# Kernel tuning notes

Hardware: AMD Instinct MI355X
Metric: run time of the kernel (lower is better)

The kernel has to match this reference:

```python
import jax, jax.numpy as jnp
import numpy as np

# Model dims (match init_kwargs)
B, S = 2, 2048          # batch, seq_len
H = 1024                # hidden_size
D = 2048                # expert_hidden_dim
E = 8                   # num_experts
K = 2                   # num_experts_per_tok (top_k)


def setup_inputs() -> dict:
    key = jax.random.key(0)
    k_x, k_g, k_w1, k_w2 = jax.random.split(key, 4)
    x = jax.random.normal(k_x, (B, S, H), jnp.float32)
    # router gate: Linear(H, E, bias=False)
    gate_w = jax.random.normal(k_g, (H, E), jnp.float32) / jnp.sqrt(H).astype(jnp.float32)
    # per-expert FFN params stacked on leading expert axis
    W1 = jax.random.normal(k_w1, (E, H, D), jnp.float32) / jnp.sqrt(H).astype(jnp.float32)
    b1 = jnp.zeros((E, D), jnp.float32)
    W2 = jax.random.normal(k_w2, (E, D, H), jnp.float32) / jnp.sqrt(D).astype(jnp.float32)
    b2 = jnp.zeros((E, H), jnp.float32)
    return {"x": x, "gate_w": gate_w, "W1": W1, "b1": b1, "W2": W2, "b2": b2}


def reference(x, gate_w, W1, b1, W2, b2):
    # --- router ---
    logits = jnp.einsum('bsh,he->bse', x, gate_w)            # [B,S,E]
    probs = jax.nn.softmax(logits, axis=-1)                  # [B,S,E]
    topk_p, idx = jax.lax.top_k(probs, K)                    # [B,S,K] each
    topk_p = topk_p / topk_p.sum(axis=-1, keepdims=True)     # renormalize over top-k
    one_hot = jax.nn.one_hot(idx, E, dtype=probs.dtype)      # [B,S,K,E]
    # combine weight per (token, expert); topk indices are distinct so this
    # equals the original's masked-sum of router_probs_flat * expert_mask
    combine = jnp.einsum('bske,bsk->bse', one_hot, topk_p)   # [B,S,E]

    # --- aux load-balancing loss (faithful to original reductions) ---
    tokens_per_expert = one_hot.sum(axis=-2).mean(axis=0)    # [S,E]
    avg_prob_per_expert = probs.mean(axis=(0, 1))            # [E]
    aux_loss = E * (tokens_per_expert * avg_prob_per_expert).sum()

    # --- experts: dense-equivalent of gather-FFN-scatter (tokens with
    # combine weight 0 contribute 0, matching the masked loop) ---
    out = jnp.zeros_like(x)
    for e in range(E):  # fixed small loop over structurally distinct experts
        h = jax.nn.gelu(jnp.einsum('bsh,hd->bsd', x, W1[e]) + b1[e], approximate=False)
        out = out + combine[..., e:e + 1] * (jnp.einsum('bsd,dh->bsh', h, W2[e]) + b2[e])
    return out, aux_loss
```

## Files before the change

### kernel.cpp

```cpp
#include <hip/hip_runtime.h>
#include <hip/hip_bf16.h>

#define NTOK 4096
#define HD   1024
#define DD   2048
#define NE   8
#define SLOTS (2*NTOK)

typedef unsigned short u16;
typedef unsigned int   u32;
typedef __attribute__((ext_vector_type(8))) __bf16 bf16x8;
typedef __attribute__((ext_vector_type(4))) float  f32x4;

__device__ __forceinline__ float bf2f(u16 u) {
    u32 v = ((u32)u) << 16;
    return __uint_as_float(v);
}
__device__ __forceinline__ u16 f2bf(float f) {
    __hip_bfloat16 h = __float2bfloat16(f);
    return *reinterpret_cast<u16*>(&h);
}

__device__ __forceinline__ void gload_lds16(const void* g, void* l) {
    __builtin_amdgcn_global_load_lds(
        (__attribute__((address_space(1))) void*)g,
        (__attribute__((address_space(3))) void*)l,
        16, 0, 0);
}

__device__ __forceinline__ float gelu_f(float v) {
    float x = 0.7978845608028654f * (v + 0.044715f * v * v * v);
    float e = exp2f(x * 2.8853900817779268f);
    float th = 1.f - 2.f * __builtin_amdgcn_rcpf(e + 1.f);
    return 0.5f * v * (1.f + th);
}

__global__ __launch_bounds__(256) void cvt2_k(
        const float* __restrict__ W1, const float* __restrict__ W2,
        u16* __restrict__ W1t, u16* __restrict__ W2t) {
    int z = blockIdx.z;
    const float* src; u16* dst; int R, C;
    if (z < NE) { src = W1 + (size_t)z * HD * DD;        dst = W1t + (size_t)z * HD * DD;        R = HD; C = DD; }
    else        { src = W2 + (size_t)(z - NE) * DD * HD; dst = W2t + (size_t)(z - NE) * DD * HD; R = DD; C = HD; }
    int tcols = C >> 6;
    int r0 = (blockIdx.x / tcols) * 64;
    int c0 = (blockIdx.x % tcols) * 64;

    __shared__ u16 tile[64][68];
    int tid = threadIdx.x;
    int rr  = tid >> 4;
    int cc4 = (tid & 15) * 4;
#pragma unroll
    for (int j = 0; j < 4; ++j) {
        int r = rr + j * 16;
        float4 v = *reinterpret_cast<const float4*>(src + (size_t)(r0 + r) * C + c0 + cc4);
        tile[r][cc4 + 0] = f2bf(v.x); tile[r][cc4 + 1] = f2bf(v.y);
        tile[r][cc4 + 2] = f2bf(v.z); tile[r][cc4 + 3] = f2bf(v.w);
    }
    __syncthreads();
    int cc = tid >> 3, sl = tid & 7;
#pragma unroll
    for (int p = 0; p < 2; ++p) {
        int c = p * 32 + cc;
        u16 tmp[8];
#pragma unroll
        for (int k = 0; k < 8; ++k) tmp[k] = tile[sl * 8 + k][c];
        *reinterpret_cast<uint4*>(dst + (size_t)(c0 + c) * R + r0 + sl * 8) =
            *reinterpret_cast<uint4*>(tmp);
    }
}

__global__ __launch_bounds__(256) void router_k(
        const float* __restrict__ x, const float* __restrict__ gw,
        u16* __restrict__ xb,
        int* __restrict__ counts, float* __restrict__ sum_probs,
        int* __restrict__ tk_idx, float* __restrict__ tk_w) {
    __shared__ int   bcnt[NE];
    __shared__ float bprob[NE];
    int tid = threadIdx.x;
    if (tid < NE) { bcnt[tid] = 0; bprob[tid] = 0.f; }
    __syncthreads();

    int gtid = blockIdx.x * 256 + tid;
    int t    = gtid >> 6;
    int lane = gtid & 63;

    float acc[NE] = {0.f,0.f,0.f,0.f,0.f,0.f,0.f,0.f};
    const float* xr = x + (size_t)t * HD;
    u16* xbr = xb + (size_t)t * HD;
#pragma unroll
    for (int i = 0; i < HD / 64; ++i) {
        int h = lane + i * 64;
        float xv = xr[h];
        xbr[h] = f2bf(xv);
        const float4* g = reinterpret_cast<const float4*>(gw + (size_t)h * NE);
        float4 g0 = g[0], g1 = g[1];
        acc[0] = fmaf(xv, g0.x, acc[0]); acc[1] = fmaf(xv, g0.y, acc[1]);
        acc[2] = fmaf(xv, g0.z, acc[2]); acc[3] = fmaf(xv, g0.w, acc[3]);
        acc[4] = fmaf(xv, g1.x, acc[4]); acc[5] = fmaf(xv, g1.y, acc[5]);
        acc[6] = fmaf(xv, g1.z, acc[6]); acc[7] = fmaf(xv, g1.w, acc[7]);
    }
#pragma unroll
    for (int off = 32; off >= 1; off >>= 1) {
#pragma unroll
        for (int e = 0; e < NE; ++e) acc[e] += __shfl_xor(acc[e], off);
    }
    float m = acc[0];
#pragma unroll
    for (int e = 1; e < NE; ++e) m = fmaxf(m, acc[e]);
    float p[NE]; float s = 0.f;
#pragma unroll
    for (int e = 0; e < NE; ++e) { p[e] = expf(acc[e] - m); s += p[e]; }
    float inv = 1.f / s;

    int i1 = 0; float v1 = p[0];
#pragma unroll
    for (int e = 1; e < NE; ++e) if (p[e] > v1) { v1 = p[e]; i1 = e; }
    int i2 = -1; float v2 = -1.f;
#pragma unroll
    for (int e = 0; e < NE; ++e) if (e != i1 && p[e] > v2) { v2 = p[e]; i2 = e; }
    float wsum = v1 + v2;

    if (lane < NE) atomicAdd(&bprob[lane], p[lane] * inv);
    if (lane == 0) {
        atomicAdd(&bcnt[i1], 1);
        atomicAdd(&bcnt[i2], 1);
        tk_idx[2 * t]     = i1;  tk_idx[2 * t + 1] = i2;
        tk_w[2 * t]       = v1 / wsum;
        tk_w[2 * t + 1]   = v2 / wsum;
    }
    __syncthreads();
    if (tid < NE) {
        if (bcnt[tid]) atomicAdd(&counts[tid], bcnt[tid]);
        atomicAdd(&sum_probs[tid], bprob[tid]);
    }
}

__global__ __launch_bounds__(256) void scatter_k(
        const int* __restrict__ tk_idx, const int* __restrict__ counts,
        int* __restrict__ cursor, int* __restrict__ slot_tok,
        int* __restrict__ inv_slot, int* __restrict__ offsets) {
    __shared__ int off[NE];
    if (threadIdx.x == 0) {
        int o = 0;
        for (int e = 0; e < NE; ++e) { off[e] = o; o += counts[e]; }
        if (blockIdx.x == 0)
            for (int e = 0; e < NE; ++e) offsets[e] = off[e];
    }
    __syncthreads();
    int t = blockIdx.x * 256 + threadIdx.x;
    if (t >= NTOK) return;
#pragma unroll
    for (int k = 0; k < 2; ++k) {
        int e = tk_idx[2 * t + k];
        int pos = atomicAdd(&cursor[e], 1);
        int s = off[e] + pos;
        slot_tok[s] = t;
        inv_slot[2 * t + k] = s;
    }
}

template<int KD, bool GATHER, bool GELU>
__global__ __launch_bounds__(256) void gemm_dense_k(
        const u16* __restrict__ A,
        const u16* __restrict__ Bt,
        const float* __restrict__ bias,
        const int* __restrict__ counts, const int* __restrict__ offsets,
        const int* __restrict__ slot_tok,
        u16* __restrict__ outb, int ND) {
    int mb = blockIdx.y;
    int e = -1, m0 = 0, accb = 0;
#pragma unroll
    for (int ee = 0; ee < NE; ++ee) {
        int nb = (counts[ee] + 127) >> 7;
        if (e < 0 && mb < accb + nb) { e = ee; m0 = (mb - accb) * 128; }
        accb += nb;
    }
    if (e < 0) return;
    int cnt = counts[e], base = offsets[e];
    int n0 = blockIdx.x * 128;

    __shared__ u16 As[128 * 64];
    __shared__ u16 Bs[128 * 64];
    __shared__ int ids[128];

    int tid  = threadIdx.x;
    int lane = tid & 63;
    int w    = tid >> 6;
    int wr   = w >> 1, wc = w & 1;
    int lrow = lane & 15, khi = lane >> 4;

    if constexpr (GATHER) {
        if (tid < 128) ids[tid] = (m0 + tid < cnt) ? slot_tok[base + m0 + tid] : 0;
    }
    __syncthreads();

    const u16* Bte = Bt + (size_t)e * (size_t)ND * KD;
    int srow = tid >> 3;
    int sslot = tid & 7;

    const u16 *gA[4], *gB[4];
#pragma unroll
    for (int j = 0; j < 4; ++j) {
        int r = j * 32 + srow;
        size_t gr;
        if constexpr (GATHER) gr = (size_t)ids[r];
        else                  gr = (size_t)(base + m0 + r);
        gA[j] = A   + gr * KD                + ((sslot ^ (r & 7)) << 3);
        gB[j] = Bte + (size_t)(n0 + r) * KD  + ((sslot ^ (r & 7)) << 3);
    }

    f32x4 acc[4][4];
#pragma unroll
    for (int m = 0; m < 4; ++m)
#pragma unroll
        for (int n = 0; n < 4; ++n) acc[m][n] = {0.f, 0.f, 0.f, 0.f};

    constexpr int NK = KD / 64;
#pragma unroll 1
    for (int t = 0; t < NK; ++t) {
#pragma unroll
        for (int j = 0; j < 4; ++j) {
            gload_lds16(gA[j] + t * 64, (char*)As + j * 4096 + tid * 16);
            gload_lds16(gB[j] + t * 64, (char*)Bs + j * 4096 + tid * 16);
        }
        __syncthreads();
#pragma unroll
        for (int ks = 0; ks < 2; ++ks) {
            int slot = ks * 4 + khi;
            bf16x8 af[4], bv[4];
#pragma unroll
            for (int m = 0; m < 4; ++m) {
                int r = wr * 64 + m * 16 + lrow;
                af[m] = *reinterpret_cast<const bf16x8*>(
                    &As[r * 64 + ((slot ^ (r & 7)) << 3)]);
            }
#pragma unroll
            for (int n = 0; n < 4; ++n) {
                int r = wc * 64 + n * 16 + lrow;
                bv[n] = *reinterpret_cast<const bf16x8*>(
                    &Bs[r * 64 + ((slot ^ (r & 7)) << 3)]);
            }
            __builtin_amdgcn_s_setprio(1);
#pragma unroll
            for (int m = 0; m < 4; ++m)
#pragma unroll
                for (int n = 0; n < 4; ++n)
                    acc[m][n] = __builtin_amdgcn_mfma_f32_16x16x32_bf16(
                        af[m], bv[n], acc[m][n], 0, 0, 0);
            __builtin_amdgcn_s_setprio(0);
        }
        __syncthreads();
    }

    constexpr int PST = 72;
    u16* patch = As + w * 16 * PST;
    float bvals[4];
    if constexpr (GELU) {
#pragma unroll
        for (int n = 0; n < 4; ++n)
            bvals[n] = bias[(size_t)e * ND + n0 + wc * 64 + n * 16 + lrow];
    }
#pragma unroll
    for (int m = 0; m < 4; ++m) {
#pragma unroll
        for (int n = 0; n < 4; ++n)
#pragma unroll
            for (int i = 0; i < 4; ++i) {
                float v = acc[m][n][i];
                if constexpr (GELU) {
                    v += bvals[n];
                    v = gelu_f(v);
                }
                patch[(khi * 4 + i) * PST + n * 16 + lrow] = f2bf(v);
            }
        __syncthreads();
        int prow = lane >> 3, sl = lane & 7;
#pragma unroll
        for (int p = 0; p < 2; ++p) {
            int row  = p * 8 + prow;
            uint4 q = *reinterpret_cast<const uint4*>(&patch[row * PST + sl * 8]);
            int grow = m0 + wr * 64 + m * 16 + row;
            if (grow < cnt)
                *reinterpret_cast<uint4*>(
                    outb + (size_t)(base + grow) * ND + n0 + wc * 64 + sl * 8) = q;
        }
        __syncthreads();
    }
}

template<int KD, bool GATHER, bool GELU>
__global__ __launch_bounds__(512) void gemm_big2_k(
        const u16* __restrict__ A,
        const u16* __restrict__ Bt,
        const float* __restrict__ bias,
        const int* __restrict__ counts, const int* __restrict__ offsets,
        const int* __restrict__ slot_tok,
        u16* __restrict__ outb, int ND) {
    int mb = blockIdx.y;
    int e = -1, m0 = 0, accb = 0;
#pragma unroll
    for (int ee = 0; ee < NE; ++ee) {
        int nb = (counts[ee] + 255) >> 8;
        if (e < 0 && mb < accb + nb) { e = ee; m0 = (mb - accb) * 256; }
        accb += nb;
    }
    if (e < 0) return;
    int cnt = counts[e], base = offsets[e];
    int n0 = blockIdx.x * 128;

    __shared__ u16 As[2][256 * 64];
    __shared__ u16 Bs[2][128 * 64];
    __shared__ int ids[256];

    int tid  = threadIdx.x;
    int lane = tid & 63;
    int w    = tid >> 6;
    int wr   = w >> 1, wc = w & 1;
    int lrow = lane & 15, khi = lane >> 4;

    if constexpr (GATHER) {
        if (tid < 256) ids[tid] = (m0 + tid < cnt) ? slot_tok[base + m0 + tid] : 0;
    }
    __syncthreads();

    const u16* Bte = Bt + (size_t)e * (size_t)ND * KD;
    int srow = tid >> 3;
    int sslot = tid & 7;

    const u16 *gA[4], *gB[2];
#pragma unroll
    for (int j = 0; j < 4; ++j) {
        int r = j * 64 + srow;
        size_t gr;
        if constexpr (GATHER) gr = (size_t)ids[r];
        else                  gr = (size_t)(base + m0 + r);
        gA[j] = A + gr * KD + ((sslot ^ (r & 7)) << 3);
    }
#pragma unroll
    for (int j = 0; j < 2; ++j) {
        int r = j * 64 + srow;
        gB[j] = Bte + (size_t)(n0 + r) * KD + ((sslot ^ (r & 7)) << 3);
    }

    f32x4 acc[4][4];
#pragma unroll
    for (int m = 0; m < 4; ++m)
#pragma unroll
        for (int n = 0; n < 4; ++n) acc[m][n] = {0.f, 0.f, 0.f, 0.f};

    auto stage = [&](int buf, int t) {
#pragma unroll
        for (int j = 0; j < 4; ++j)
            gload_lds16(gA[j] + t * 64, (char*)As[buf] + j * 8192 + tid * 16);
#pragma unroll
        for (int j = 0; j < 2; ++j)
            gload_lds16(gB[j] + t * 64, (char*)Bs[buf] + j * 8192 + tid * 16);
    };
    auto compute = [&](int buf) {
#pragma unroll
        for (int ks = 0; ks < 2; ++ks) {
            int slot = ks * 4 + khi;
            bf16x8 af[4], bv[4];
#pragma unroll
            for (int m = 0; m < 4; ++m) {
                int r = wr * 64 + m * 16 + lrow;
                af[m] = *reinterpret_cast<const bf16x8*>(
                    &As[buf][r * 64 + ((slot ^ (r & 7)) << 3)]);
            }
#pragma unroll
            for (int n = 0; n < 4; ++n) {
                int r = wc * 64 + n * 16 + lrow;
                bv[n] = *reinterpret_cast<const bf16x8*>(
                    &Bs[buf][r * 64 + ((slot ^ (r & 7)) << 3)]);
            }
            __builtin_amdgcn_s_setprio(1);
#pragma unroll
            for (int m = 0; m < 4; ++m)
#pragma unroll
                for (int n = 0; n < 4; ++n)
                    acc[m][n] = __builtin_amdgcn_mfma_f32_16x16x32_bf16(
                        af[m], bv[n], acc[m][n], 0, 0, 0);
            __builtin_amdgcn_s_setprio(0);
        }
    };

    constexpr int NK = KD / 64;
    stage(0, 0);
    __syncthreads();
#pragma unroll 1
    for (int t = 0; t < NK; ++t) {
        if (t + 1 < NK) stage((t + 1) & 1, t + 1);
        compute(t & 1);
        __syncthreads();
    }

    constexpr int PST = 72;
    u16* patch = ((u16*)As) + w * 16 * PST;
    float bvals[4];
    if constexpr (GELU) {
#pragma unroll
        for (int n = 0; n < 4; ++n)
            bvals[n] = bias[(size_t)e * ND + n0 + wc * 64 + n * 16 + lrow];
    }
#pragma unroll
    for (int m = 0; m < 4; ++m) {
#pragma unroll
        for (int n = 0; n < 4; ++n)
#pragma unroll
            for (int i = 0; i < 4; ++i) {
                float v = acc[m][n][i];
                if constexpr (GELU) {
                    v += bvals[n];
                    v = gelu_f(v);
                }
                patch[(khi * 4 + i) * PST + n * 16 + lrow] = f2bf(v);
            }
        __syncthreads();
        int prow = lane >> 3, sl = lane & 7;
#pragma unroll
        for (int p = 0; p < 2; ++p) {
            int row  = p * 8 + prow;
            uint4 q = *reinterpret_cast<const uint4*>(&patch[row * PST + sl * 8]);
            int grow = m0 + wr * 64 + m * 16 + row;
            if (grow < cnt)
                *reinterpret_cast<uint4*>(
                    outb + (size_t)(base + grow) * ND + n0 + wc * 64 + sl * 8) = q;
        }
        __syncthreads();
    }
}

__global__ __launch_bounds__(256) void combine_k(
        const int* __restrict__ tk_idx, const float* __restrict__ tk_w,
        const int* __restrict__ inv_slot, const u16* __restrict__ ybuf,
        const float* __restrict__ b2, float* __restrict__ out) {
    int gtid = blockIdx.x * 256 + threadIdx.x;
    int t = gtid >> 6;
    int lane = gtid & 63;
    int e0 = tk_idx[2 * t], e1 = tk_idx[2 * t + 1];
    float w0 = tk_w[2 * t], w1 = tk_w[2 * t + 1];
    int s0 = inv_slot[2 * t], s1 = inv_slot[2 * t + 1];

#pragma unroll
    for (int i = 0; i < 2; ++i) {
        int c = lane * 8 + i * 512;
        uint4 q0 = *reinterpret_cast<const uint4*>(ybuf + (size_t)s0 * HD + c);
        uint4 q1 = *reinterpret_cast<const uint4*>(ybuf + (size_t)s1 * HD + c);
        float y0[8] = {bf2f((u16)(q0.x&0xffff)), bf2f((u16)(q0.x>>16)),
                       bf2f((u16)(q0.y&0xffff)), bf2f((u16)(q0.y>>16)),
                       bf2f((u16)(q0.z&0xffff)), bf2f((u16)(q0.z>>16)),
                       bf2f((u16)(q0.w&0xffff)), bf2f((u16)(q0.w>>16))};
        float y1[8] = {bf2f((u16)(q1.x&0xffff)), bf2f((u16)(q1.x>>16)),
                       bf2f((u16)(q1.y&0xffff)), bf2f((u16)(q1.y>>16)),
                       bf2f((u16)(q1.z&0xffff)), bf2f((u16)(q1.z>>16)),
                       bf2f((u16)(q1.w&0xffff)), bf2f((u16)(q1.w>>16))};
        float r[8];
#pragma unroll
        for (int j = 0; j < 8; ++j) {
            float v0 = y0[j] + b2[e0 * HD + c + j];
            float v1 = y1[j] + b2[e1 * HD + c + j];
            r[j] = w0 * v0 + w1 * v1;
        }
        float* op = out + (size_t)t * HD + c;
        *reinterpret_cast<float4*>(op)     = make_float4(r[0], r[1], r[2], r[3]);
        *reinterpret_cast<float4*>(op + 4) = make_float4(r[4], r[5], r[6], r[7]);
    }
}

__global__ void finalize_k(const int* __restrict__ counts,
                           const float* __restrict__ sum_probs,
                           float* __restrict__ out_aux) {
    if (threadIdx.x == 0) {
        double s = 0.0;
        for (int e = 0; e < NE; ++e) s += (double)counts[e] * (double)sum_probs[e];
        out_aux[0] = (float)(s * (8.0 / (2.0 * (double)NTOK)));
    }
}

extern "C" void kernel_launch(void* const* d_in, const int* in_sizes, int n_in,
                              void* d_out, int out_size, void* d_ws, size_t ws_size,
                              hipStream_t stream) {
    const float* x   = (const float*)d_in[0];
    const float* gw  = (const float*)d_in[1];
    const float* W1  = (const float*)d_in[2];
    const float* b1  = (const float*)d_in[3];
    const float* W2  = (const float*)d_in[4];
    const float* b2  = (const float*)d_in[5];
    float* out = (float*)d_out;

    char* ws = (char*)d_ws;
    int*   counts    = (int*)(ws + 0);
    int*   cursor    = (int*)(ws + 32);
    int*   offsets   = (int*)(ws + 64);
    float* sum_probs = (float*)(ws + 128);
    int*   tk_idx    = (int*)(ws + 512);
    float* tk_w      = (float*)(ws + 33280);
    int*   slot_tok  = (int*)(ws + 66048);
    int*   inv_slot  = (int*)(ws + 98816);
    u16*   xb        = (u16*)(ws + 131584);
    u16*   W1t       = (u16*)(ws + 8520192);
    u16*   W2t       = (u16*)(ws + 42074624);
    u16*   hbuf      = (u16*)(ws + 75629056);
    u16*   ybuf      = W1t;

    hipMemsetAsync(ws, 0, 512, stream);

    cvt2_k<<<dim3(512, 1, 2 * NE), 256, 0, stream>>>(W1, W2, W1t, W2t);
    router_k<<<NTOK / 4, 256, 0, stream>>>(x, gw, xb, counts, sum_probs, tk_idx, tk_w);
    scatter_k<<<NTOK / 256, 256, 0, stream>>>(tk_idx, counts, cursor,
                                              slot_tok, inv_slot, offsets);

    gemm_dense_k<HD, true, true><<<dim3(DD / 128, 72, 1), 256, 0, stream>>>(
        xb, W1t, b1, counts, offsets, slot_tok, hbuf, DD);
    gemm_big2_k<DD, false, false><<<dim3(HD / 128, 40, 1), 512, 0, stream>>>(
        hbuf, W2t, nullptr, counts, offsets, slot_tok, ybuf, HD);

    combine_k<<<NTOK / 4, 256, 0, stream>>>(tk_idx, tk_w, inv_slot, ybuf, b2, out);
    finalize_k<<<1, 64, 0, stream>>>(counts, sum_probs, out + (size_t)NTOK * HD);
}
```

Before: 247.1 us.

## Replace second expert GEMM with smaller 128x64 single-buffered tile kernel

The second expert GEMM moves from 256x128 tiles with 512 threads and double-buffered LDS to 128x64 tiles with 256 threads and a single LDS buffer. The grid grows from 40x8 to 72x16 blocks, giving more blocks to fill the GPU's compute units. The cost is lower data reuse per block and no overlap of global loads with MFMA work. The separate finalize kernel is also folded into combine_k to save one launch.

```diff
diff --git a/kernel.cpp b/kernel.cpp
--- a/kernel.cpp
+++ b/kernel.cpp
@@ -289,29 +289,26 @@
     }
 }
 
-template<int KD, bool GATHER, bool GELU>
-__global__ __launch_bounds__(512) void gemm_big2_k(
+template<int KD>
+__global__ __launch_bounds__(256) void gemm_n64_k(
         const u16* __restrict__ A,
         const u16* __restrict__ Bt,
-        const float* __restrict__ bias,
         const int* __restrict__ counts, const int* __restrict__ offsets,
-        const int* __restrict__ slot_tok,
         u16* __restrict__ outb, int ND) {
     int mb = blockIdx.y;
     int e = -1, m0 = 0, accb = 0;
 #pragma unroll
     for (int ee = 0; ee < NE; ++ee) {
-        int nb = (counts[ee] + 255) >> 8;
-        if (e < 0 && mb < accb + nb) { e = ee; m0 = (mb - accb) * 256; }
+        int nb = (counts[ee] + 127) >> 7;
+        if (e < 0 && mb < accb + nb) { e = ee; m0 = (mb - accb) * 128; }
         accb += nb;
     }
     if (e < 0) return;
     int cnt = counts[e], base = offsets[e];
-    int n0 = blockIdx.x * 128;
-
-    __shared__ u16 As[2][256 * 64];
-    __shared__ u16 Bs[2][128 * 64];
-    __shared__ int ids[256];
+    int n0 = blockIdx.x * 64;
+
+    __shared__ u16 As[128 * 64];
+    __shared__ u16 Bs[64 * 64];
 
     int tid  = threadIdx.x;
     int lane = tid & 63;
@@ -319,11 +316,6 @@
     int wr   = w >> 1, wc = w & 1;
     int lrow = lane & 15, khi = lane >> 4;
 
-    if constexpr (GATHER) {
-        if (tid < 256) ids[tid] = (m0 + tid < cnt) ? slot_tok[base + m0 + tid] : 0;
-    }
-    __syncthreads();
-
     const u16* Bte = Bt + (size_t)e * (size_t)ND * KD;
     int srow = tid >> 3;
     int sslot = tid & 7;
@@ -331,102 +323,75 @@
     const u16 *gA[4], *gB[2];
 #pragma unroll
     for (int j = 0; j < 4; ++j) {
-        int r = j * 64 + srow;
-        size_t gr;
-        if constexpr (GATHER) gr = (size_t)ids[r];
-        else                  gr = (size_t)(base + m0 + r);
-        gA[j] = A + gr * KD + ((sslot ^ (r & 7)) << 3);
+        int r = j * 32 + srow;
+        gA[j] = A + (size_t)(base + m0 + r) * KD + ((sslot ^ (r & 7)) << 3);
     }
 #pragma unroll
     for (int j = 0; j < 2; ++j) {
-        int r = j * 64 + srow;
+        int r = j * 32 + srow;
         gB[j] = Bte + (size_t)(n0 + r) * KD + ((sslot ^ (r & 7)) << 3);
     }
 
-    f32x4 acc[4][4];
+    f32x4 acc[4][2];
 #pragma unroll
     for (int m = 0; m < 4; ++m)
 #pragma unroll
-        for (int n = 0; n < 4; ++n) acc[m][n] = {0.f, 0.f, 0.f, 0.f};
-
-    auto stage = [&](int buf, int t) {
+        for (int n = 0; n < 2; ++n) acc[m][n] = {0.f, 0.f, 0.f, 0.f};
+
+    constexpr int NK = KD / 64;
+#pragma unroll 1
+    for (int t = 0; t < NK; ++t) {
 #pragma unroll
         for (int j = 0; j < 4; ++j)
-            gload_lds16(gA[j] + t * 64, (char*)As[buf] + j * 8192 + tid * 16);
+            gload_lds16(gA[j] + t * 64, (char*)As + j * 4096 + tid * 16);
 #pragma unroll
         for (int j = 0; j < 2; ++j)
-            gload_lds16(gB[j] + t * 64, (char*)Bs[buf] + j * 8192 + tid * 16);
-    };
-    auto compute = [&](int buf) {
+            gload_lds16(gB[j] + t * 64, (char*)Bs + j * 4096 + tid * 16);
+        __syncthreads();
 #pragma unroll
         for (int ks = 0; ks < 2; ++ks) {
             int slot = ks * 4 + khi;
-            bf16x8 af[4], bv[4];
+            bf16x8 af[4], bv[2];
 #pragma unroll
             for (int m = 0; m < 4; ++m) {
                 int r = wr * 64 + m * 16 + lrow;
                 af[m] = *reinterpret_cast<const bf16x8*>(
-                    &As[buf][r * 64 + ((slot ^ (r & 7)) << 3)]);
+                    &As[r * 64 + ((slot ^ (r & 7)) << 3)]);
             }
 #pragma unroll
-            for (int n = 0; n < 4; ++n) {
-                int r = wc * 64 + n * 16 + lrow;
+            for (int n = 0; n < 2; ++n) {
+                int r = wc * 32 + n * 16 + lrow;
                 bv[n] = *reinterpret_cast<const bf16x8*>(
-                    &Bs[buf][r * 64 + ((slot ^ (r & 7)) << 3)]);
+                    &Bs[r * 64 + ((slot ^ (r & 7)) << 3)]);
             }
             __builtin_amdgcn_s_setprio(1);
 #pragma unroll
             for (int m = 0; m < 4; ++m)
 #pragma unroll
-                for (int n = 0; n < 4; ++n)
+                for (int n = 0; n < 2; ++n)
                     acc[m][n] = __builtin_amdgcn_mfma_f32_16x16x32_bf16(
                         af[m], bv[n], acc[m][n], 0, 0, 0);
             __builtin_amdgcn_s_setprio(0);
         }
-    };
-
-    constexpr int NK = KD / 64;
-    stage(0, 0);
-    __syncthreads();
-#pragma unroll 1
-    for (int t = 0; t < NK; ++t) {
-        if (t + 1 < NK) stage((t + 1) & 1, t + 1);
-        compute(t & 1);
-        __syncthreads();
-    }
-
-    constexpr int PST = 72;
-    u16* patch = ((u16*)As) + w * 16 * PST;
-    float bvals[4];
-    if constexpr (GELU) {
-#pragma unroll
-        for (int n = 0; n < 4; ++n)
-            bvals[n] = bias[(size_t)e * ND + n0 + wc * 64 + n * 16 + lrow];
-    }
+        __syncthreads();
+    }
+
+    constexpr int PST = 40;
+    u16* patch = As + w * 16 * PST;
 #pragma unroll
     for (int m = 0; m < 4; ++m) {
 #pragma unroll
-        for (int n = 0; n < 4; ++n)
-#pragma unroll
-            for (int i = 0; i < 4; ++i) {
-                float v = acc[m][n][i];
-                if constexpr (GELU) {
-                    v += bvals[n];
-                    v = gelu_f(v);
-                }
-                patch[(khi * 4 + i) * PST + n * 16 + lrow] = f2bf(v);
-            }
-        __syncthreads();
-        int prow = lane >> 3, sl = lane & 7;
-#pragma unroll
-        for (int p = 0; p < 2; ++p) {
-            int row  = p * 8 + prow;
-            uint4 q = *reinterpret_cast<const uint4*>(&patch[row * PST + sl * 8]);
-            int grow = m0 + wr * 64 + m * 16 + row;
-            if (grow < cnt)
-                *reinterpret_cast<uint4*>(
-                    outb + (size_t)(base + grow) * ND + n0 + wc * 64 + sl * 8) = q;
-        }
+        for (int n = 0; n < 2; ++n)
+#pragma unroll
+            for (int i = 0; i < 4; ++i)
+                patch[(khi * 4 + i) * PST + n * 16 + lrow] = f2bf(acc[m][n][i]);
+        __syncthreads();
+        int row = lane >> 2, sl = lane & 3;
+        uint4 q = *reinterpret_cast<const uint4*>(&patch[row * PST + sl * 8]);
+        int grow = m0 + wr * 64 + m * 16 + row;
+        if (grow < cnt)
+            *reinterpret_cast<uint4*>(
+                outb + (size_t)(base + grow) * ND + n0 + wc * 32 + sl * 8) = q;
         __syncthreads();
     }
 }
@@ -434,7 +399,14 @@
 __global__ __launch_bounds__(256) void combine_k(
         const int* __restrict__ tk_idx, const float* __restrict__ tk_w,
         const int* __restrict__ inv_slot, const u16* __restrict__ ybuf,
-        const float* __restrict__ b2, float* __restrict__ out) {
+        const float* __restrict__ b2, float* __restrict__ out,
+        const int* __restrict__ counts, const float* __restrict__ sum_probs,
+        float* __restrict__ out_aux) {
+    if (blockIdx.x == 0 && threadIdx.x == 0) {
+        double s = 0.0;
+        for (int e = 0; e < NE; ++e) s += (double)counts[e] * (double)sum_probs[e];
+        out_aux[0] = (float)(s * (8.0 / (2.0 * (double)NTOK)));
+    }
     int gtid = blockIdx.x * 256 + threadIdx.x;
     int t = gtid >> 6;
     int lane = gtid & 63;
@@ -465,16 +437,6 @@
         float* op = out + (size_t)t * HD + c;
         *reinterpret_cast<float4*>(op)     = make_float4(r[0], r[1], r[2], r[3]);
         *reinterpret_cast<float4*>(op + 4) = make_float4(r[4], r[5], r[6], r[7]);
-    }
-}
-
-__global__ void finalize_k(const int* __restrict__ counts,
-                           const float* __restrict__ sum_probs,
-                           float* __restrict__ out_aux) {
-    if (threadIdx.x == 0) {
-        double s = 0.0;
-        for (int e = 0; e < NE; ++e) s += (double)counts[e] * (double)sum_probs[e];
-        out_aux[0] = (float)(s * (8.0 / (2.0 * (double)NTOK)));
     }
 }
 
@@ -513,9 +475,10 @@
 
     gemm_dense_k<HD, true, true><<<dim3(DD / 128, 72, 1), 256, 0, stream>>>(
         xb, W1t, b1, counts, offsets, slot_tok, hbuf, DD);
-    gemm_big2_k<DD, false, false><<<dim3(HD / 128, 40, 1), 512, 0, stream>>>(
-        hbuf, W2t, nullptr, counts, offsets, slot_tok, ybuf, HD);
-
-    combine_k<<<NTOK / 4, 256, 0, stream>>>(tk_idx, tk_w, inv_slot, ybuf, b2, out);
-    finalize_k<<<1, 64, 0, stream>>>(counts, sum_probs, out + (size_t)NTOK * HD);
-}
+    gemm_n64_k<DD><<<dim3(HD / 64, 72, 1), 256, 0, stream>>>(
+        hbuf, W2t, counts, offsets, ybuf, HD);
+
+    combine_k<<<NTOK / 4, 256, 0, stream>>>(tk_idx, tk_w, inv_slot, ybuf, b2, out,
+                                            counts, sum_probs,
+                                            out + (size_t)NTOK * HD);
+}
```

Measured after the change: 215.4 us. 12.8% less time.
